# Optimization experiments

Measured on AMD Instinct MI355X. Metric: run time of the kernel, lower is better.

## Reference

```python
import jax, jax.numpy as jnp
import numpy as np

BN_EPS = 1e-5

def batch_norm(x, gamma, beta):
    # training-mode BatchNorm1d: biased batch stats over the edge dim
    mean = jnp.mean(x, axis=0)
    var = jnp.var(x, axis=0)
    return (x - mean) * jax.lax.rsqrt(var + BN_EPS) * gamma + beta

def setup_inputs() -> dict:
    key = jax.random.key(0)
    ks = jax.random.split(key, 10)
    N, F, E = 50000, 128, 600000
    D_in = 2 * F + 12  # 268
    h = jax.random.normal(ks[0], (N, F), dtype=jnp.float32)
    edge_feature = jax.random.normal(ks[1], (E, 12), dtype=jnp.float32)
    src = jax.random.randint(ks[2], (E,), 0, N)
    dst = jax.random.randint(ks[3], (E,), 0, N)
    def lin(k, fan_in, shape):
        bound = 1.0 / np.sqrt(fan_in)
        return jax.random.uniform(k, shape, jnp.float32, -bound, bound)
    W1 = lin(ks[4], D_in, (28, D_in)); b1 = lin(ks[5], D_in, (28,))
    W2 = lin(ks[6], 28, (8, 28));      b2 = lin(ks[7], 28, (8,))
    W3 = lin(ks[8], 8, (1, 8));        b3 = lin(ks[9], 8, (1,))
    gamma1 = jnp.ones((28,), jnp.float32); beta1 = jnp.zeros((28,), jnp.float32)
    gamma2 = jnp.ones((8,), jnp.float32);  beta2 = jnp.zeros((8,), jnp.float32)
    return {"h": h, "edge_feature": edge_feature, "src": src, "dst": dst,
            "W1": W1, "b1": b1, "gamma1": gamma1, "beta1": beta1,
            "W2": W2, "b2": b2, "gamma2": gamma2, "beta2": beta2,
            "W3": W3, "b3": b3}

def reference(h, edge_feature, src, dst, W1, b1, gamma1, beta1,
              W2, b2, gamma2, beta2, W3, b3):
    h_u = h[src]                    # [E, F] gather of source node feats
    h_v = h[dst]                    # [E, F] gather of dest node feats
    x = jnp.concatenate([h_u, h_v, edge_feature], axis=1)  # [E, 2F+12]
    s = jax.nn.relu(batch_norm(x @ W1.T + b1, gamma1, beta1))  # [E, 28]
    s = jax.nn.relu(batch_norm(s @ W2.T + b2, gamma2, beta2))  # [E, 8]
    score = s @ W3.T + b3           # [E, 1]
    return score
```

## Files before the change

### kernel.cpp

```cpp
#include <hip/hip_runtime.h>

#define BN_EPS 1e-5f
typedef unsigned short u16;
typedef unsigned int u32;


__device__ __forceinline__ u16 f2bf(float f) {
  u32 u = __float_as_uint(f);
  return (u16)((u + 0x7fffu + ((u >> 16) & 1u)) >> 16);
}
__device__ __forceinline__ float bf2f(u16 s) {
  return __uint_as_float(((u32)s) << 16);
}
__device__ __forceinline__ u32 pack2(float a, float b) {
  return (u32)f2bf(a) | ((u32)f2bf(b) << 16);
}

__global__ void k1_proj(const float* __restrict__ h, const float* __restrict__ W1,
                        u16* __restrict__ Psrc, u16* __restrict__ Pdst,
                        float* __restrict__ stats, int N) {
  if (blockIdx.x == 0 && threadIdx.x < 72) stats[threadIdx.x] = 0.f;
  const int half = blockIdx.x & 1;
  const int node = (blockIdx.x >> 1) * 256 + threadIdx.x;
  if (node >= N) return;
  const float* __restrict__ wbase = W1 + half * 128;
  const float4* __restrict__ h4 = (const float4*)(h + (size_t)node * 128);
  float acc[28];
#pragma unroll
  for (int c = 0; c < 28; c++) acc[c] = 0.f;
  for (int kk = 0; kk < 16; kk++) {
    const float4 a = h4[kk * 2];
    const float4 b = h4[kk * 2 + 1];
#pragma unroll
    for (int c = 0; c < 28; c++) {
      const float* w = wbase + c * 268 + kk * 8;
      acc[c] += a.x * w[0] + a.y * w[1] + a.z * w[2] + a.w * w[3]
              + b.x * w[4] + b.y * w[5] + b.z * w[6] + b.w * w[7];
    }
  }
  u16* outp = (half == 0 ? Psrc : Pdst) + (size_t)node * 32;
  u32 u[14];
#pragma unroll
  for (int j = 0; j < 14; j++) u[j] = pack2(acc[2 * j], acc[2 * j + 1]);
  uint4* p4 = (uint4*)outp;
  p4[0] = make_uint4(u[0], u[1], u[2], u[3]);
  p4[1] = make_uint4(u[4], u[5], u[6], u[7]);
  p4[2] = make_uint4(u[8], u[9], u[10], u[11]);
  *(uint2*)((u32*)outp + 12) = make_uint2(u[12], u[13]);
}

__global__ void __launch_bounds__(256) k2_l1(
    const u16* __restrict__ Psrc, const u16* __restrict__ Pdst,
    const float* __restrict__ ef,
    const int* __restrict__ src, const int* __restrict__ dst,
    const float* __restrict__ W1, const float* __restrict__ b1,
    u16* __restrict__ y1, float* __restrict__ stats, int E, int epw) {
  const int tid = threadIdx.x;
  const int lane = tid & 63;
  const int c = lane & 31;
  const int g = tid >> 5;
  const int G = blockIdx.x * 8 + g;
  int e0 = G * epw;
  int e1 = e0 + epw;
  if (e1 > E) e1 = E;
  if (e0 > e1) e0 = e1;

  const bool act = (c < 28);
  float w[12];
#pragma unroll
  for (int j = 0; j < 12; j++) w[j] = 0.f;
  float bias = 0.f;
  if (act) {
    const float4* wp = (const float4*)(W1 + c * 268 + 256);
    float4 w0 = wp[0], w1 = wp[1], w2 = wp[2];
    w[0] = w0.x; w[1] = w0.y; w[2] = w0.z; w[3] = w0.w;
    w[4] = w1.x; w[5] = w1.y; w[6] = w1.z; w[7] = w1.w;
    w[8] = w2.x; w[9] = w2.y; w[10] = w2.z; w[11] = w2.w;
    bias = b1[c];
  }

  float sum = 0.f, ssq = 0.f;
  int e = e0;
  for (; e + 4 <= e1; e += 4) {
    const int4 sI = *(const int4*)(src + e);
    const int4 dI = *(const int4*)(dst + e);
    float pa[4], pb[4];
    pa[0] = bf2f(Psrc[(size_t)(u32)sI.x * 32 + c]);
    pa[1] = bf2f(Psrc[(size_t)(u32)sI.y * 32 + c]);
    pa[2] = bf2f(Psrc[(size_t)(u32)sI.z * 32 + c]);
    pa[3] = bf2f(Psrc[(size_t)(u32)sI.w * 32 + c]);
    pb[0] = bf2f(Pdst[(size_t)(u32)dI.x * 32 + c]);
    pb[1] = bf2f(Pdst[(size_t)(u32)dI.y * 32 + c]);
    pb[2] = bf2f(Pdst[(size_t)(u32)dI.z * 32 + c]);
    pb[3] = bf2f(Pdst[(size_t)(u32)dI.w * 32 + c]);
    float4 f0[4], f1[4], f2[4];
#pragma unroll
    for (int k = 0; k < 4; k++) {
      const float4* e4 = (const float4*)(ef + (size_t)(e + k) * 12);
      f0[k] = e4[0]; f1[k] = e4[1]; f2[k] = e4[2];
    }
#pragma unroll
    for (int k = 0; k < 4; k++) {
      float y = bias;
      y = fmaf(f0[k].x, w[0], y); y = fmaf(f0[k].y, w[1], y);
      y = fmaf(f0[k].z, w[2], y); y = fmaf(f0[k].w, w[3], y);
      y = fmaf(f1[k].x, w[4], y); y = fmaf(f1[k].y, w[5], y);
      y = fmaf(f1[k].z, w[6], y); y = fmaf(f1[k].w, w[7], y);
      y = fmaf(f2[k].x, w[8], y); y = fmaf(f2[k].y, w[9], y);
      y = fmaf(f2[k].z, w[10], y); y = fmaf(f2[k].w, w[11], y);
      y += pa[k] + pb[k];
      if (act) {
        sum += y;
        ssq += y * y;
        y1[(size_t)(e + k) * 28 + c] = f2bf(y);
      }
    }
  }
  for (; e < e1; e++) {
    const int sI = src[e], dI = dst[e];
    const float pa = bf2f(Psrc[(size_t)(u32)sI * 32 + c]);
    const float pb = bf2f(Pdst[(size_t)(u32)dI * 32 + c]);
    const float4* e4 = (const float4*)(ef + (size_t)e * 12);
    float4 f0 = e4[0], f1 = e4[1], f2 = e4[2];
    float y = bias;
    y = fmaf(f0.x, w[0], y); y = fmaf(f0.y, w[1], y);
    y = fmaf(f0.z, w[2], y); y = fmaf(f0.w, w[3], y);
    y = fmaf(f1.x, w[4], y); y = fmaf(f1.y, w[5], y);
    y = fmaf(f1.z, w[6], y); y = fmaf(f1.w, w[7], y);
    y = fmaf(f2.x, w[8], y); y = fmaf(f2.y, w[9], y);
    y = fmaf(f2.z, w[10], y); y = fmaf(f2.w, w[11], y);
    y += pa + pb;
    if (act) {
      sum += y;
      ssq += y * y;
      y1[(size_t)e * 28 + c] = f2bf(y);
    }
  }

  sum += __shfl_xor(sum, 32);
  ssq += __shfl_xor(ssq, 32);
  __shared__ float red[2][4][28];
  const int wave = tid >> 6;
  if (lane < 28) { red[0][wave][lane] = sum; red[1][wave][lane] = ssq; }
  __syncthreads();
  if (tid < 28) {
    atomicAdd(&stats[tid], red[0][0][tid] + red[0][1][tid] + red[0][2][tid] + red[0][3][tid]);
    atomicAdd(&stats[28 + tid], red[1][0][tid] + red[1][1][tid] + red[1][2][tid] + red[1][3][tid]);
  }
}

__global__ void __launch_bounds__(256) k4_l2(
    const u32* __restrict__ y1w, const float* __restrict__ stats,
    const float* __restrict__ g1, const float* __restrict__ be1,
    const float* __restrict__ W2, const float* __restrict__ b2,
    u16* __restrict__ y2, float* __restrict__ stats2, int E, float invE) {
  __shared__ u32 tile[256 * 15];
  float sc[28], sh[28];
#pragma unroll
  for (int cc = 0; cc < 28; cc++) {
    const float m = stats[cc] * invE;
    const float v = stats[28 + cc] * invE - m * m;
    const float s = g1[cc] * rsqrtf(v + BN_EPS);
    sc[cc] = s; sh[cc] = be1[cc] - m * s;
  }
  float as[8], aq[8];
#pragma unroll
  for (int o = 0; o < 8; o++) { as[o] = 0.f; aq[o] = 0.f; }
  const int tid = threadIdx.x;
  for (int T = blockIdx.x * 256; T < E; T += gridDim.x * 256) {
    int cnt = E - T; if (cnt > 256) cnt = 256;
    __syncthreads();
    const int total = cnt * 14;
    for (int i = tid; i < total; i += 256) {
      const int r = i / 14, j = i - r * 14;
      tile[r * 15 + j] = __builtin_nontemporal_load(&y1w[(size_t)T * 14 + i]);
    }
    __syncthreads();
    if (tid < cnt) {
      u32 uu[14];
#pragma unroll
      for (int i = 0; i < 14; i++) uu[i] = tile[tid * 15 + i];
      float acc[8];
#pragma unroll
      for (int o = 0; o < 8; o++) acc[o] = b2[o];
#pragma unroll
      for (int k = 0; k < 14; k++) {
        const float fe = __uint_as_float(uu[k] << 16);
        const float fo = __uint_as_float(uu[k] & 0xffff0000u);
        const float se = fmaxf(fmaf(fe, sc[2 * k], sh[2 * k]), 0.f);
        const float so = fmaxf(fmaf(fo, sc[2 * k + 1], sh[2 * k + 1]), 0.f);
#pragma unroll
        for (int o = 0; o < 8; o++) {
          acc[o] = fmaf(W2[o * 28 + 2 * k], se, acc[o]);
          acc[o] = fmaf(W2[o * 28 + 2 * k + 1], so, acc[o]);
        }
      }
      *(uint4*)(y2 + (size_t)(T + tid) * 8) =
          make_uint4(pack2(acc[0], acc[1]), pack2(acc[2], acc[3]),
                     pack2(acc[4], acc[5]), pack2(acc[6], acc[7]));
#pragma unroll
      for (int o = 0; o < 8; o++) { as[o] += acc[o]; aq[o] += acc[o] * acc[o]; }
    }
  }
#pragma unroll
  for (int o = 0; o < 8; o++) {
    for (int off = 32; off; off >>= 1) {
      as[o] += __shfl_down(as[o], off);
      aq[o] += __shfl_down(aq[o], off);
    }
  }
  __shared__ float redS[4][16];
  const int wave = tid >> 6, lane = tid & 63;
  if (lane == 0) {
#pragma unroll
    for (int o = 0; o < 8; o++) { redS[wave][o] = as[o]; redS[wave][8 + o] = aq[o]; }
  }
  __syncthreads();
  if (tid < 16) {
    atomicAdd(&stats2[tid], redS[0][tid] + redS[1][tid] + redS[2][tid] + redS[3][tid]);
  }
}

__global__ void k6_l3(const u16* __restrict__ y2, const float* __restrict__ stats,
                      const float* __restrict__ g2, const float* __restrict__ be2,
                      const float* __restrict__ W3, const float* __restrict__ b3,
                      float* __restrict__ out, int E, float invE) {
  float sc[8], sh[8], w3[8];
#pragma unroll
  for (int o = 0; o < 8; o++) {
    const float m = stats[56 + o] * invE;
    const float v = stats[64 + o] * invE - m * m;
    const float s = g2[o] * rsqrtf(v + BN_EPS);
    sc[o] = s; sh[o] = be2[o] - m * s; w3[o] = W3[o];
  }
  const int e = blockIdx.x * blockDim.x + threadIdx.x;
  if (e >= E) return;
  const uint4 r = *(const uint4*)(y2 + (size_t)e * 8);
  u32 uu[4] = {r.x, r.y, r.z, r.w};
  float acc = b3[0];
#pragma unroll
  for (int k = 0; k < 4; k++) {
    const float fe = __uint_as_float(uu[k] << 16);
    const float fo = __uint_as_float(uu[k] & 0xffff0000u);
    acc = fmaf(w3[2 * k], fmaxf(fmaf(fe, sc[2 * k], sh[2 * k]), 0.f), acc);
    acc = fmaf(w3[2 * k + 1], fmaxf(fmaf(fo, sc[2 * k + 1], sh[2 * k + 1]), 0.f), acc);
  }
  out[e] = acc;
}

extern "C" void kernel_launch(void* const* d_in, const int* in_sizes, int n_in,
                              void* d_out, int out_size, void* d_ws, size_t ws_size,
                              hipStream_t stream) {
  const float* h   = (const float*)d_in[0];
  const float* ef  = (const float*)d_in[1];
  const int* src   = (const int*)d_in[2];
  const int* dst   = (const int*)d_in[3];
  const float* W1  = (const float*)d_in[4];
  const float* b1  = (const float*)d_in[5];
  const float* g1  = (const float*)d_in[6];
  const float* be1 = (const float*)d_in[7];
  const float* W2  = (const float*)d_in[8];
  const float* b2  = (const float*)d_in[9];
  const float* g2  = (const float*)d_in[10];
  const float* be2 = (const float*)d_in[11];
  const float* W3  = (const float*)d_in[12];
  const float* b3  = (const float*)d_in[13];
  float* out = (float*)d_out;

  const int N = in_sizes[0] / 128;
  const int E = in_sizes[2];
  const float invE = 1.0f / (float)E;

  char* ws = (char*)d_ws;
  float* stats = (float*)ws;
  u16* Psrc = (u16*)(ws + 1024);
  u16* Pdst = Psrc + (size_t)N * 32;
  u16* y1   = Pdst + (size_t)N * 32;
  u16* y2   = y1 + (size_t)E * 28;

  const int nodeBlocks = (N + 255) / 256;
  k1_proj<<<nodeBlocks * 2, 256, 0, stream>>>(h, W1, Psrc, Pdst, stats, N);

  const int K2B = 2048;
  int epw = (E + K2B * 8 - 1) / (K2B * 8);
  epw = (epw + 7) & ~7;
  k2_l1<<<K2B, 256, 0, stream>>>(Psrc, Pdst, ef, src, dst, W1, b1, y1, stats, E, epw);

  const int K4B = (E + 255) / 256;
  k4_l2<<<K4B, 256, 0, stream>>>((const u32*)y1, stats, g1, be1, W2, b2, y2,
                                 stats + 56, E, invE);
  k6_l3<<<(E + 255) / 256, 256, 0, stream>>>(y2, stats, g2, be2, W3, b3, out, E, invE);
}
```

Baseline: 304.2 us.

## Restructure node projection to keep W1 rows in registers per lane

The node projection kernel now maps one output channel to each wavefront lane (56 lanes covering the src and dst halves) and keeps that lane's 128 W1 weights in registers. Each wavefront then loops over a contiguous range of nodes, so weights are loaded once instead of being re-read per node. The layer-2 kernel drops its nontemporal load hint and launches a quarter as many blocks, relying on its grid-stride loop. The new mapping broadcasts the h row to all lanes and uses 128 weight registers per thread, which may lower occupancy, and it writes bf16 outputs as scattered 2-byte stores.

After: 314.0 us. 1.03x slower.

```diff
diff --git a/kernel.cpp b/kernel.cpp
--- a/kernel.cpp
+++ b/kernel.cpp
@@ -16,37 +16,36 @@
   return (u32)f2bf(a) | ((u32)f2bf(b) << 16);
 }
 
-__global__ void k1_proj(const float* __restrict__ h, const float* __restrict__ W1,
-                        u16* __restrict__ Psrc, u16* __restrict__ Pdst,
-                        float* __restrict__ stats, int N) {
+__global__ void __launch_bounds__(256) k1_proj(
+    const float* __restrict__ h, const float* __restrict__ W1,
+    u16* __restrict__ Psrc, u16* __restrict__ Pdst,
+    float* __restrict__ stats, int N, int npw) {
   if (blockIdx.x == 0 && threadIdx.x < 72) stats[threadIdx.x] = 0.f;
-  const int half = blockIdx.x & 1;
-  const int node = (blockIdx.x >> 1) * 256 + threadIdx.x;
-  if (node >= N) return;
-  const float* __restrict__ wbase = W1 + half * 128;
-  const float4* __restrict__ h4 = (const float4*)(h + (size_t)node * 128);
-  float acc[28];
-#pragma unroll
-  for (int c = 0; c < 28; c++) acc[c] = 0.f;
-  for (int kk = 0; kk < 16; kk++) {
-    const float4 a = h4[kk * 2];
-    const float4 b = h4[kk * 2 + 1];
-#pragma unroll
-    for (int c = 0; c < 28; c++) {
-      const float* w = wbase + c * 268 + kk * 8;
-      acc[c] += a.x * w[0] + a.y * w[1] + a.z * w[2] + a.w * w[3]
-              + b.x * w[4] + b.y * w[5] + b.z * w[6] + b.w * w[7];
-    }
-  }
-  u16* outp = (half == 0 ? Psrc : Pdst) + (size_t)node * 32;
-  u32 u[14];
-#pragma unroll
-  for (int j = 0; j < 14; j++) u[j] = pack2(acc[2 * j], acc[2 * j + 1]);
-  uint4* p4 = (uint4*)outp;
-  p4[0] = make_uint4(u[0], u[1], u[2], u[3]);
-  p4[1] = make_uint4(u[4], u[5], u[6], u[7]);
-  p4[2] = make_uint4(u[8], u[9], u[10], u[11]);
-  *(uint2*)((u32*)outp + 12) = make_uint2(u[12], u[13]);
+  const int tid = threadIdx.x;
+  const int lane = tid & 63;
+  const int wid = (blockIdx.x * 256 + tid) >> 6;
+  const int c = (lane < 56) ? lane : 55;
+  const float* wrow = (c < 28) ? (W1 + c * 268) : (W1 + (c - 28) * 268 + 128);
+  float4 wreg[32];
+#pragma unroll
+  for (int q = 0; q < 32; q++) wreg[q] = ((const float4*)wrow)[q];
+
+  int n0 = wid * npw;
+  int n1 = n0 + npw;
+  if (n1 > N) n1 = N;
+  if (n0 > n1) n0 = n1;
+  for (int n = n0; n < n1; n++) {
+    const float4* h4 = (const float4*)(h + (size_t)n * 128);
+    float acc = 0.f;
+#pragma unroll
+    for (int q = 0; q < 32; q++) {
+      const float4 a = h4[q];
+      acc += a.x * wreg[q].x + a.y * wreg[q].y + a.z * wreg[q].z + a.w * wreg[q].w;
+    }
+    const u16 v = f2bf(acc);
+    if (lane < 28)      Psrc[(size_t)n * 32 + lane] = v;
+    else if (lane < 56) Pdst[(size_t)n * 32 + (lane - 28)] = v;
+  }
 }
 
 __global__ void __launch_bounds__(256) k2_l1(
@@ -173,7 +172,7 @@
     const int total = cnt * 14;
     for (int i = tid; i < total; i += 256) {
       const int r = i / 14, j = i - r * 14;
-      tile[r * 15 + j] = __builtin_nontemporal_load(&y1w[(size_t)T * 14 + i]);
+      tile[r * 15 + j] = y1w[(size_t)T * 14 + i];
     }
     __syncthreads();
     if (tid < cnt) {
@@ -278,15 +277,16 @@
   u16* y1   = Pdst + (size_t)N * 32;
   u16* y2   = y1 + (size_t)E * 28;
 
-  const int nodeBlocks = (N + 255) / 256;
-  k1_proj<<<nodeBlocks * 2, 256, 0, stream>>>(h, W1, Psrc, Pdst, stats, N);
+  const int K1B = 512;
+  const int npw = (N + K1B * 4 - 1) / (K1B * 4);
+  k1_proj<<<K1B, 256, 0, stream>>>(h, W1, Psrc, Pdst, stats, N, npw);
 
   const int K2B = 2048;
   int epw = (E + K2B * 8 - 1) / (K2B * 8);
   epw = (epw + 7) & ~7;
   k2_l1<<<K2B, 256, 0, stream>>>(Psrc, Pdst, ef, src, dst, W1, b1, y1, stats, E, epw);
 
-  const int K4B = (E + 255) / 256;
+  const int K4B = (E + 1023) / 1024;
   k4_l2<<<K4B, 256, 0, stream>>>((const u32*)y1, stats, g1, be1, W2, b2, y2,
                                  stats + 56, E, invE);
   k6_l3<<<(E + 255) / 256, 256, 0, stream>>>(y2, stats, g2, be2, W3, b3, out, E, invE);
```
